# Kernel optimization log

Measured on AMD Instinct MI355X. Metric: run time of the kernel, lower is better.

Reference implementation:

```python
import jax, jax.numpy as jnp
import numpy as np

N_NODES = 100000
N_EDGES = 1600000
IN_DIM, HID_DIM, OUT_DIM = 128, 32, 32
NEG_SLOPE = 0.2  # DGL GATConv default


def setup_inputs() -> dict:
    key = jax.random.key(0)
    ks = jax.random.split(key, 12)
    features = jax.random.normal(ks[0], (N_NODES, IN_DIM), dtype=jnp.float32)
    src = jax.random.randint(ks[1], (N_EDGES,), 0, N_NODES, dtype=jnp.int32)
    dst = jax.random.randint(ks[2], (N_EDGES,), 0, N_NODES, dtype=jnp.int32)
    s1 = 1.0 / np.sqrt(IN_DIM)
    s2 = 1.0 / np.sqrt(HID_DIM)
    W1 = jax.random.normal(ks[3], (IN_DIM, HID_DIM), dtype=jnp.float32) * s1
    al1 = jax.random.normal(ks[4], (HID_DIM,), dtype=jnp.float32) * s2
    ar1 = jax.random.normal(ks[5], (HID_DIM,), dtype=jnp.float32) * s2
    b1 = jnp.zeros((HID_DIM,), dtype=jnp.float32)
    W2 = jax.random.normal(ks[6], (HID_DIM, OUT_DIM), dtype=jnp.float32) * s2
    al2 = jax.random.normal(ks[7], (OUT_DIM,), dtype=jnp.float32) * s2
    ar2 = jax.random.normal(ks[8], (OUT_DIM,), dtype=jnp.float32) * s2
    b2 = jnp.zeros((OUT_DIM,), dtype=jnp.float32)
    return {"features": features, "src": src, "dst": dst,
            "W1": W1, "al1": al1, "ar1": ar1, "b1": b1,
            "W2": W2, "al2": al2, "ar2": ar2, "b2": b2}


def gat_conv(x, W, a_l, a_r, b, src, dst, n_nodes):
    # x: [N, Din] -> h: [N, D]
    h = x @ W
    el = h @ a_l  # [N] per-node left attention logit
    er = h @ a_r  # [N]
    # per-edge score with LeakyReLU (DGL default negative_slope=0.2)
    e = jax.nn.leaky_relu(el[src] + er[dst], negative_slope=NEG_SLOPE)  # [E]
    # segment softmax over edges grouped by destination node
    emax = jax.ops.segment_max(e, dst, num_segments=n_nodes)  # [N]
    ex = jnp.exp(e - emax[dst])  # [E]
    denom = jax.ops.segment_sum(ex, dst, num_segments=n_nodes)  # [N]
    alpha = ex / denom[dst]  # [E], every edge's dst has degree >= 1
    # scatter-weighted aggregation of source features
    out = jax.ops.segment_sum(h[src] * alpha[:, None], dst, num_segments=n_nodes)
    return out + b


def reference(features, src, dst, W1, al1, ar1, b1, W2, al2, ar2, b2):
    n = features.shape[0]
    h = gat_conv(features, W1, al1, ar1, b1, src, dst, n)
    h = jax.nn.elu(h)
    out = gat_conv(h, W2, al2, ar2, b2, src, dst, n)
    return out  # [N, OUT_DIM]
```

## Files before the change

### kernel.cpp

```cpp
#include <hip/hip_runtime.h>
#include <hip/hip_bf16.h>

#define N_NODES 100000
#define N_EDGES 1600000
#define IN_DIM 128
#define HID 32
#define BW 128
#define NBUCK ((N_NODES + BW - 1) / BW)
#define CAP 4096


using bf16x8 = __attribute__((ext_vector_type(8))) short;
using f32x4  = __attribute__((ext_vector_type(4))) float;

__device__ __forceinline__ short f2bf(float f) {
    return __builtin_bit_cast(short, __float2bfloat16(f));
}
__device__ __forceinline__ float bf2f(short s) {
    return __bfloat162float(__builtin_bit_cast(__hip_bfloat16, s));
}

__global__ __launch_bounds__(256) void gemm1_kernel(
    const float* __restrict__ x, const float* __restrict__ W,
    const float* __restrict__ al, const float* __restrict__ ar,
    __hip_bfloat16* __restrict__ h, float* __restrict__ el, float* __restrict__ er,
    int* __restrict__ gcur)
{
    __shared__ float Xs[64][132];
    const int tid = threadIdx.x;
    const int row0 = blockIdx.x * 64;

    const int gid = blockIdx.x * 256 + tid;
    if (gid < NBUCK) gcur[gid] = gid * CAP;

    const int lane = tid & 63, wid = tid >> 6;
    const int l15 = lane & 15, g = lane >> 4;

    bf16x8 bh[4][2], bl[4][2];
    #pragma unroll
    for (int q = 0; q < 4; ++q)
        #pragma unroll
        for (int ct = 0; ct < 2; ++ct)
            #pragma unroll
            for (int j = 0; j < 8; ++j) {
                const float wv = W[(32 * q + 8 * g + j) * HID + ct * 16 + l15];
                const short hi = f2bf(wv);
                bh[q][ct][j] = hi;
                bl[q][ct][j] = f2bf(wv - bf2f(hi));
            }

    #pragma unroll
    for (int i = 0; i < 8; ++i) {
        const int f = tid + 256 * i;
        const int r = f >> 5, c4 = f & 31;
        const int gr = row0 + r;
        float4 v = make_float4(0.f, 0.f, 0.f, 0.f);
        if (gr < N_NODES) v = ((const float4*)x)[(size_t)gr * 32 + c4];
        *(float4*)&Xs[r][c4 * 4] = v;
    }
    __syncthreads();

    const int tile = blockIdx.x * 4 + wid;
    if (tile * 16 >= N_NODES) return;
    const int rl = wid * 16 + l15;

    f32x4 acc0 = {0.f, 0.f, 0.f, 0.f}, acc1 = {0.f, 0.f, 0.f, 0.f};
    #pragma unroll
    for (int q = 0; q < 4; ++q) {
        const float4 xa = *(const float4*)&Xs[rl][32 * q + 8 * g];
        const float4 xb = *(const float4*)&Xs[rl][32 * q + 8 * g + 4];
        const float xs[8] = {xa.x, xa.y, xa.z, xa.w, xb.x, xb.y, xb.z, xb.w};
        bf16x8 ah, alo;
        #pragma unroll
        for (int j = 0; j < 8; ++j) {
            const short hi = f2bf(xs[j]);
            ah[j] = hi;
            alo[j] = f2bf(xs[j] - bf2f(hi));
        }
        acc0 = __builtin_amdgcn_mfma_f32_16x16x32_bf16(ah,  bh[q][0], acc0, 0, 0, 0);
        acc0 = __builtin_amdgcn_mfma_f32_16x16x32_bf16(alo, bh[q][0], acc0, 0, 0, 0);
        acc0 = __builtin_amdgcn_mfma_f32_16x16x32_bf16(ah,  bl[q][0], acc0, 0, 0, 0);
        acc1 = __builtin_amdgcn_mfma_f32_16x16x32_bf16(ah,  bh[q][1], acc1, 0, 0, 0);
        acc1 = __builtin_amdgcn_mfma_f32_16x16x32_bf16(alo, bh[q][1], acc1, 0, 0, 0);
        acc1 = __builtin_amdgcn_mfma_f32_16x16x32_bf16(ah,  bl[q][1], acc1, 0, 0, 0);
    }

    const int grow0 = tile * 16 + 4 * g;
    const float a0 = al[l15], a1 = al[16 + l15];
    const float r0 = ar[l15], r1 = ar[16 + l15];
    float pel[4], per_[4];
    #pragma unroll
    for (int i = 0; i < 4; ++i) {
        const int grow = grow0 + i;
        h[(size_t)grow * HID + l15]      = __float2bfloat16(acc0[i]);
        h[(size_t)grow * HID + 16 + l15] = __float2bfloat16(acc1[i]);
        pel[i]  = acc0[i] * a0 + acc1[i] * a1;
        per_[i] = acc0[i] * r0 + acc1[i] * r1;
    }
    #pragma unroll
    for (int m = 1; m < 16; m <<= 1)
        #pragma unroll
        for (int i = 0; i < 4; ++i) {
            pel[i]  += __shfl_xor(pel[i],  m, 16);
            per_[i] += __shfl_xor(per_[i], m, 16);
        }
    if (l15 == 0)
        #pragma unroll
        for (int i = 0; i < 4; ++i) { el[grow0 + i] = pel[i]; er[grow0 + i] = per_[i]; }
}

__global__ __launch_bounds__(512) void bin_kernel(const int* __restrict__ src,
                                                  const int* __restrict__ dst,
                                                  int* __restrict__ gcur,
                                                  int* __restrict__ pairs)
{
    __shared__ int hist[NBUCK];
    __shared__ int cur[NBUCK];
    const int tid = threadIdx.x;
    for (int i = tid; i < NBUCK; i += 512) hist[i] = 0;
    __syncthreads();

    const int t = blockIdx.x * 512 + tid;
    const bool act = t < N_EDGES / 16;
    int4 sv[4], dv[4];
    if (act) {
        const int4* s4 = (const int4*)src + (size_t)t * 4;
        const int4* d4 = (const int4*)dst + (size_t)t * 4;
        #pragma unroll
        for (int q = 0; q < 4; ++q) { sv[q] = s4[q]; dv[q] = d4[q]; }
        #pragma unroll
        for (int q = 0; q < 4; ++q) {
            atomicAdd(&hist[dv[q].x >> 7], 1); atomicAdd(&hist[dv[q].y >> 7], 1);
            atomicAdd(&hist[dv[q].z >> 7], 1); atomicAdd(&hist[dv[q].w >> 7], 1);
        }
    }
    __syncthreads();
    for (int i = tid; i < NBUCK; i += 512) {
        const int hv = hist[i];
        cur[i] = hv ? atomicAdd(&gcur[i], hv) : 0;
    }
    __syncthreads();
    if (act) {
        #pragma unroll
        for (int q = 0; q < 4; ++q) {
            const int ss[4] = {sv[q].x, sv[q].y, sv[q].z, sv[q].w};
            const int dd[4] = {dv[q].x, dv[q].y, dv[q].z, dv[q].w};
            #pragma unroll
            for (int r = 0; r < 4; ++r) {
                const int slot = atomicAdd(&cur[dd[r] >> 7], 1);
                pairs[slot] = (ss[r] << 7) | (dd[r] & (BW - 1));
            }
        }
    }
}

__global__ __launch_bounds__(256) void lsort_kernel(
    const int* __restrict__ gcur, int* __restrict__ pairs,
    const float* __restrict__ el, const float* __restrict__ er,
    int* __restrict__ deg, int* __restrict__ rowptr, float* __restrict__ w1)
{
    __shared__ int lp[CAP];
    __shared__ int lc[CAP];
    __shared__ int lhist[BW];
    __shared__ int lcur[BW];
    __shared__ float ers[BW];
    __shared__ int w0tot;
    const int tid = threadIdx.x;
    const int b = blockIdx.x;
    const int rbase = b * CAP;
    const int node0 = b * BW;
    int ecnt = gcur[b] - rbase;
    if (ecnt > CAP) ecnt = CAP;
    if (tid < BW) {
        lhist[tid] = 0;
        ers[tid] = (node0 + tid < N_NODES) ? er[node0 + tid] : 0.f;
    }
    __syncthreads();
    for (int i = tid; i < ecnt; i += 256) {
        const int p = pairs[rbase + i];
        lp[i] = p;
        atomicAdd(&lhist[p & (BW - 1)], 1);
    }
    __syncthreads();
    const int lane = tid & 63;
    int v = 0;
    if (tid < BW) v = lhist[tid];
    int pre = v;
    #pragma unroll
    for (int off = 1; off < 64; off <<= 1) {
        const int n = __shfl_up(pre, off, 64);
        if (lane >= off) pre += n;
    }
    if (tid == 63) w0tot = pre;
    __syncthreads();
    if (tid < BW) {
        const int ex = pre - v + (tid >= 64 ? w0tot : 0);
        lcur[tid] = ex;
        const int node = node0 + tid;
        if (node < N_NODES) { deg[node] = v; rowptr[node] = rbase + ex; }
    }
    __syncthreads();
    for (int i = tid; i < ecnt; i += 256) {
        const int p = lp[i];
        const int slot = atomicAdd(&lcur[p & (BW - 1)], 1);
        lc[slot] = p;
    }
    __syncthreads();
    for (int i = tid; i < ecnt; i += 256) {
        const int p = lc[i];
        pairs[rbase + i] = p;
        float sc = el[p >> 7] + ers[p & (BW - 1)];
        sc = sc > 0.f ? sc : 0.2f * sc;
        w1[rbase + i] = __expf(sc);
    }
}

__global__ __launch_bounds__(256) void wcalc_kernel(
    const int* __restrict__ gcur, const int* __restrict__ csr,
    const float* __restrict__ el, const float* __restrict__ er,
    float* __restrict__ w)
{
    __shared__ float ers[BW];
    const int tid = threadIdx.x;
    const int b = blockIdx.x;
    const int rbase = b * CAP;
    const int node0 = b * BW;
    if (tid < BW) ers[tid] = (node0 + tid < N_NODES) ? er[node0 + tid] : 0.f;
    __syncthreads();
    int ecnt = gcur[b] - rbase;
    if (ecnt > CAP) ecnt = CAP;
    for (int i = tid; i < ecnt; i += 256) {
        const int p = csr[rbase + i];
        float sc = el[p >> 7] + ers[p & (BW - 1)];
        sc = sc > 0.f ? sc : 0.2f * sc;
        w[rbase + i] = __expf(sc);
    }
}

template <int MODE>
__global__ __launch_bounds__(256) void gather_kernel(
    const int* __restrict__ rowptr, const int* __restrict__ deg,
    const int* __restrict__ csr, const float* __restrict__ w,
    const __hip_bfloat16* __restrict__ h, const float* __restrict__ bias,
    const float* __restrict__ W2, const float* __restrict__ al2,
    const float* __restrict__ ar2,
    __hip_bfloat16* __restrict__ h2, float* __restrict__ el2,
    float* __restrict__ er2, float* __restrict__ out)
{
    const int tid = threadIdx.x;
    float* W2s = nullptr;
    if constexpr (MODE == 0) {
        __shared__ float W2s_[HID * HID];
        W2s = W2s_;
        ((float4*)W2s)[tid] = ((const float4*)W2)[tid];
        __syncthreads();
    }
    const int node = blockIdx.x * 8 + (tid >> 5);
    const int col = tid & 31;
    const int cnt = deg[node];
    const int start = rowptr[node];
    float acc = 0.f, den = 0.f;
    int j = 0;
    for (; j + 7 < cnt; j += 8) {
        const int p0 = csr[start + j];
        const int p1 = csr[start + j + 1];
        const int p2 = csr[start + j + 2];
        const int p3 = csr[start + j + 3];
        const int p4 = csr[start + j + 4];
        const int p5 = csr[start + j + 5];
        const int p6 = csr[start + j + 6];
        const int p7 = csr[start + j + 7];
        const float w0 = w[start + j];
        const float w1v = w[start + j + 1];
        const float w2v = w[start + j + 2];
        const float w3v = w[start + j + 3];
        const float w4v = w[start + j + 4];
        const float w5v = w[start + j + 5];
        const float w6v = w[start + j + 6];
        const float w7v = w[start + j + 7];
        const float h0 = __bfloat162float(h[(size_t)(p0 >> 7) * HID + col]);
        const float h1 = __bfloat162float(h[(size_t)(p1 >> 7) * HID + col]);
        const float h2v = __bfloat162float(h[(size_t)(p2 >> 7) * HID + col]);
        const float h3 = __bfloat162float(h[(size_t)(p3 >> 7) * HID + col]);
        const float h4 = __bfloat162float(h[(size_t)(p4 >> 7) * HID + col]);
        const float h5 = __bfloat162float(h[(size_t)(p5 >> 7) * HID + col]);
        const float h6 = __bfloat162float(h[(size_t)(p6 >> 7) * HID + col]);
        const float h7 = __bfloat162float(h[(size_t)(p7 >> 7) * HID + col]);
        den += ((w0 + w1v) + (w2v + w3v)) + ((w4v + w5v) + (w6v + w7v));
        acc += (w0 * h0 + w1v * h1 + w2v * h2v + w3v * h3)
             + (w4v * h4 + w5v * h5 + w6v * h6 + w7v * h7);
    }
    for (; j < cnt; ++j) {
        const int p = csr[start + j];
        const float wv = w[start + j];
        den += wv;
        acc += wv * __bfloat162float(h[(size_t)(p >> 7) * HID + col]);
    }

    float v = den > 0.f ? acc / den : 0.f;
    v += bias[col];
    if constexpr (MODE == 0) {
        v = v > 0.f ? v : expm1f(v);
        float hacc = 0.f;
        #pragma unroll
        for (int k = 0; k < HID; ++k)
            hacc += __shfl(v, k, 32) * W2s[k * HID + col];
        h2[(size_t)node * HID + col] = __float2bfloat16(hacc);
        float pel = hacc * al2[col], per = hacc * ar2[col];
        #pragma unroll
        for (int mm = 16; mm > 0; mm >>= 1) {
            pel += __shfl_xor(pel, mm, 32);
            per += __shfl_xor(per, mm, 32);
        }
        if (col == 0) { el2[node] = pel; er2[node] = per; }
    } else {
        out[(size_t)node * HID + col] = v;
    }
}

extern "C" void kernel_launch(void* const* d_in, const int* in_sizes, int n_in,
                              void* d_out, int out_size, void* d_ws, size_t ws_size,
                              hipStream_t stream) {
    const float* features = (const float*)d_in[0];
    const int*   src      = (const int*)d_in[1];
    const int*   dst      = (const int*)d_in[2];
    const float* W1       = (const float*)d_in[3];
    const float* al1      = (const float*)d_in[4];
    const float* ar1      = (const float*)d_in[5];
    const float* b1       = (const float*)d_in[6];
    const float* W2       = (const float*)d_in[7];
    const float* al2      = (const float*)d_in[8];
    const float* ar2      = (const float*)d_in[9];
    const float* b2       = (const float*)d_in[10];
    float* out = (float*)d_out;

    int*  gcur   = (int*)d_ws;
    int*  deg    = gcur + 784;
    int*  rowptr = deg + N_NODES;
    int*  pairs  = rowptr + N_NODES;
    float* wbuf  = (float*)(pairs + NBUCK * CAP);
    __hip_bfloat16* h1 = (__hip_bfloat16*)(wbuf + NBUCK * CAP);
    float* el1 = (float*)(h1 + (size_t)N_NODES * HID);
    float* er1 = el1 + N_NODES;
    __hip_bfloat16* h2 = (__hip_bfloat16*)(er1 + N_NODES);
    float* el2 = (float*)(h2 + (size_t)N_NODES * HID);
    float* er2 = el2 + N_NODES;

    const int NB_E16 = (N_EDGES / 16 + 511) / 512;
    const int NB_G1  = (N_NODES + 63) / 64;

    gemm1_kernel<<<NB_G1, 256, 0, stream>>>(features, W1, al1, ar1,
                                            h1, el1, er1, gcur);
    bin_kernel<<<NB_E16, 512, 0, stream>>>(src, dst, gcur, pairs);
    lsort_kernel<<<NBUCK, 256, 0, stream>>>(gcur, pairs, el1, er1,
                                            deg, rowptr, wbuf);
    gather_kernel<0><<<N_NODES / 8, 256, 0, stream>>>(rowptr, deg, pairs, wbuf,
                                                      h1, b1, W2, al2, ar2,
                                                      h2, el2, er2, nullptr);
    wcalc_kernel<<<NBUCK, 256, 0, stream>>>(gcur, pairs, el2, er2, wbuf);
    gather_kernel<1><<<N_NODES / 8, 256, 0, stream>>>(rowptr, deg, pairs, wbuf,
                                                      h2, b2,
                                                      nullptr, nullptr, nullptr,
                                                      nullptr, nullptr, nullptr, out);
}
```

Before: 255.9 us.

## Stage binned edges in LDS for coalesced writes; split layer-2 GEMM into separate kernel

bin_kernel now sorts each block's 4096 edges into buckets in shared memory, using a wave-level prefix scan for local offsets, then writes them out contiguously per bucket. This is meant to replace scattered global writes with more coalesced ones. The ELU plus W2 projection is moved out of the first gather into a separate gemm2_kernel that goes through an fp32 intermediate buffer x2, which adds a launch and extra global traffic. The gather unroll also drops from 8 to 4.

```diff
diff --git a/kernel.cpp b/kernel.cpp
--- a/kernel.cpp
+++ b/kernel.cpp
@@ -109,18 +109,21 @@
         for (int i = 0; i < 4; ++i) { el[grow0 + i] = pel[i]; er[grow0 + i] = per_[i]; }
 }
 
-__global__ __launch_bounds__(512) void bin_kernel(const int* __restrict__ src,
+__global__ __launch_bounds__(256) void bin_kernel(const int* __restrict__ src,
                                                   const int* __restrict__ dst,
                                                   int* __restrict__ gcur,
                                                   int* __restrict__ pairs)
 {
+    __shared__ int   lp[4096];
+    __shared__ short lb[4096];
     __shared__ int hist[NBUCK];
-    __shared__ int cur[NBUCK];
-    const int tid = threadIdx.x;
-    for (int i = tid; i < NBUCK; i += 512) hist[i] = 0;
-    __syncthreads();
-
-    const int t = blockIdx.x * 512 + tid;
+    __shared__ int lcur[NBUCK];
+    __shared__ int gbase[NBUCK];
+    const int tid = threadIdx.x;
+    for (int i = tid; i < NBUCK; i += 256) hist[i] = 0;
+    __syncthreads();
+
+    const int t = blockIdx.x * 256 + tid;
     const bool act = t < N_EDGES / 16;
     int4 sv[4], dv[4];
     if (act) {
@@ -135,9 +138,24 @@
         }
     }
     __syncthreads();
-    for (int i = tid; i < NBUCK; i += 512) {
+    if (tid < 64) {
+        int carry = 0;
+        for (int c = 0; c < (NBUCK + 63) / 64; ++c) {
+            const int i = c * 64 + tid;
+            const int v = (i < NBUCK) ? hist[i] : 0;
+            int pre = v;
+            #pragma unroll
+            for (int off = 1; off < 64; off <<= 1) {
+                const int n = __shfl_up(pre, off, 64);
+                if (tid >= off) pre += n;
+            }
+            if (i < NBUCK) lcur[i] = carry + pre - v;
+            carry += __shfl(pre, 63, 64);
+        }
+    }
+    for (int i = tid; i < NBUCK; i += 256) {
         const int hv = hist[i];
-        cur[i] = hv ? atomicAdd(&gcur[i], hv) : 0;
+        gbase[i] = hv ? atomicAdd(&gcur[i], hv) : 0;
     }
     __syncthreads();
     if (act) {
@@ -147,10 +165,19 @@
             const int dd[4] = {dv[q].x, dv[q].y, dv[q].z, dv[q].w};
             #pragma unroll
             for (int r = 0; r < 4; ++r) {
-                const int slot = atomicAdd(&cur[dd[r] >> 7], 1);
-                pairs[slot] = (ss[r] << 7) | (dd[r] & (BW - 1));
+                const int b = dd[r] >> 7;
+                const int slot = atomicAdd(&lcur[b], 1);
+                lp[slot] = (ss[r] << 7) | (dd[r] & (BW - 1));
+                lb[slot] = (short)b;
             }
         }
+    }
+    __syncthreads();
+    const int ecB = min(N_EDGES - blockIdx.x * 4096, 4096);
+    for (int i = tid; i < ecB; i += 256) {
+        const int b = lb[i];
+        const int local = i - (lcur[b] - hist[b]);
+        pairs[gbase[b] + local] = lp[i];
     }
 }
 
@@ -242,53 +269,30 @@
     const int* __restrict__ rowptr, const int* __restrict__ deg,
     const int* __restrict__ csr, const float* __restrict__ w,
     const __hip_bfloat16* __restrict__ h, const float* __restrict__ bias,
-    const float* __restrict__ W2, const float* __restrict__ al2,
-    const float* __restrict__ ar2,
-    __hip_bfloat16* __restrict__ h2, float* __restrict__ el2,
-    float* __restrict__ er2, float* __restrict__ out)
-{
-    const int tid = threadIdx.x;
-    float* W2s = nullptr;
-    if constexpr (MODE == 0) {
-        __shared__ float W2s_[HID * HID];
-        W2s = W2s_;
-        ((float4*)W2s)[tid] = ((const float4*)W2)[tid];
-        __syncthreads();
-    }
+    float* __restrict__ out)
+{
+    const int tid = threadIdx.x;
     const int node = blockIdx.x * 8 + (tid >> 5);
     const int col = tid & 31;
     const int cnt = deg[node];
     const int start = rowptr[node];
     float acc = 0.f, den = 0.f;
     int j = 0;
-    for (; j + 7 < cnt; j += 8) {
+    for (; j + 3 < cnt; j += 4) {
         const int p0 = csr[start + j];
         const int p1 = csr[start + j + 1];
         const int p2 = csr[start + j + 2];
         const int p3 = csr[start + j + 3];
-        const int p4 = csr[start + j + 4];
-        const int p5 = csr[start + j + 5];
-        const int p6 = csr[start + j + 6];
-        const int p7 = csr[start + j + 7];
         const float w0 = w[start + j];
         const float w1v = w[start + j + 1];
         const float w2v = w[start + j + 2];
         const float w3v = w[start + j + 3];
-        const float w4v = w[start + j + 4];
-        const float w5v = w[start + j + 5];
-        const float w6v = w[start + j + 6];
-        const float w7v = w[start + j + 7];
         const float h0 = __bfloat162float(h[(size_t)(p0 >> 7) * HID + col]);
         const float h1 = __bfloat162float(h[(size_t)(p1 >> 7) * HID + col]);
         const float h2v = __bfloat162float(h[(size_t)(p2 >> 7) * HID + col]);
         const float h3 = __bfloat162float(h[(size_t)(p3 >> 7) * HID + col]);
-        const float h4 = __bfloat162float(h[(size_t)(p4 >> 7) * HID + col]);
-        const float h5 = __bfloat162float(h[(size_t)(p5 >> 7) * HID + col]);
-        const float h6 = __bfloat162float(h[(size_t)(p6 >> 7) * HID + col]);
-        const float h7 = __bfloat162float(h[(size_t)(p7 >> 7) * HID + col]);
-        den += ((w0 + w1v) + (w2v + w3v)) + ((w4v + w5v) + (w6v + w7v));
-        acc += (w0 * h0 + w1v * h1 + w2v * h2v + w3v * h3)
-             + (w4v * h4 + w5v * h5 + w6v * h6 + w7v * h7);
+        den += (w0 + w1v) + (w2v + w3v);
+        acc += w0 * h0 + w1v * h1 + w2v * h2v + w3v * h3;
     }
     for (; j < cnt; ++j) {
         const int p = csr[start + j];
@@ -296,26 +300,55 @@
         den += wv;
         acc += wv * __bfloat162float(h[(size_t)(p >> 7) * HID + col]);
     }
-
     float v = den > 0.f ? acc / den : 0.f;
     v += bias[col];
-    if constexpr (MODE == 0) {
-        v = v > 0.f ? v : expm1f(v);
-        float hacc = 0.f;
-        #pragma unroll
-        for (int k = 0; k < HID; ++k)
-            hacc += __shfl(v, k, 32) * W2s[k * HID + col];
-        h2[(size_t)node * HID + col] = __float2bfloat16(hacc);
-        float pel = hacc * al2[col], per = hacc * ar2[col];
-        #pragma unroll
-        for (int mm = 16; mm > 0; mm >>= 1) {
-            pel += __shfl_xor(pel, mm, 32);
-            per += __shfl_xor(per, mm, 32);
-        }
-        if (col == 0) { el2[node] = pel; er2[node] = per; }
-    } else {
-        out[(size_t)node * HID + col] = v;
-    }
+    if (MODE == 0) v = v > 0.f ? v : expm1f(v);
+    out[(size_t)node * HID + col] = v;
+}
+
+__global__ __launch_bounds__(256) void gemm2_kernel(
+    const float* __restrict__ x2, const float* __restrict__ W,
+    const float* __restrict__ al, const float* __restrict__ ar,
+    __hip_bfloat16* __restrict__ h, float* __restrict__ el, float* __restrict__ er)
+{
+    __shared__ float Ws[HID][36];
+    __shared__ float Xs[32][36];
+    const int tid = threadIdx.x;
+    const int row0 = blockIdx.x * 32;
+    {
+        const float4 wv = ((const float4*)W)[tid];
+        *(float4*)&Ws[tid >> 3][(tid & 7) * 4] = wv;
+        const float4 xv = ((const float4*)x2)[(size_t)row0 * 8 + tid];
+        *(float4*)&Xs[tid >> 3][(tid & 7) * 4] = xv;
+    }
+    __syncthreads();
+
+    const int r = tid >> 3, cg = tid & 7;
+    const int row = row0 + r;
+    float ax = 0.f, ay = 0.f, az = 0.f, aw = 0.f;
+    #pragma unroll
+    for (int k = 0; k < HID; ++k) {
+        const float xv = Xs[r][k];
+        const float4 wv = *(const float4*)&Ws[k][cg * 4];
+        ax += xv * wv.x; ay += xv * wv.y; az += xv * wv.z; aw += xv * wv.w;
+    }
+
+    ushort4 hp;
+    hp.x = __builtin_bit_cast(unsigned short, __float2bfloat16(ax));
+    hp.y = __builtin_bit_cast(unsigned short, __float2bfloat16(ay));
+    hp.z = __builtin_bit_cast(unsigned short, __float2bfloat16(az));
+    hp.w = __builtin_bit_cast(unsigned short, __float2bfloat16(aw));
+    *(ushort4*)&h[(size_t)row * HID + cg * 4] = hp;
+
+    const int c0 = cg * 4;
+    float pel = ax * al[c0] + ay * al[c0 + 1] + az * al[c0 + 2] + aw * al[c0 + 3];
+    float per = ax * ar[c0] + ay * ar[c0 + 1] + az * ar[c0 + 2] + aw * ar[c0 + 3];
+    #pragma unroll
+    for (int m = 1; m < 8; m <<= 1) {
+        pel += __shfl_xor(pel, m, 8);
+        per += __shfl_xor(per, m, 8);
+    }
+    if (cg == 0) { el[row] = pel; er[row] = per; }
 }
 
 extern "C" void kernel_launch(void* const* d_in, const int* in_sizes, int n_in,
@@ -342,24 +375,23 @@
     __hip_bfloat16* h1 = (__hip_bfloat16*)(wbuf + NBUCK * CAP);
     float* el1 = (float*)(h1 + (size_t)N_NODES * HID);
     float* er1 = el1 + N_NODES;
-    __hip_bfloat16* h2 = (__hip_bfloat16*)(er1 + N_NODES);
+    float* x2  = er1 + N_NODES;
+    __hip_bfloat16* h2 = (__hip_bfloat16*)(x2 + (size_t)N_NODES * HID);
     float* el2 = (float*)(h2 + (size_t)N_NODES * HID);
     float* er2 = el2 + N_NODES;
 
-    const int NB_E16 = (N_EDGES / 16 + 511) / 512;
+    const int NB_E16 = (N_EDGES / 16 + 255) / 256;
     const int NB_G1  = (N_NODES + 63) / 64;
 
     gemm1_kernel<<<NB_G1, 256, 0, stream>>>(features, W1, al1, ar1,
                                             h1, el1, er1, gcur);
-    bin_kernel<<<NB_E16, 512, 0, stream>>>(src, dst, gcur, pairs);
+    bin_kernel<<<NB_E16, 256, 0, stream>>>(src, dst, gcur, pairs);
     lsort_kernel<<<NBUCK, 256, 0, stream>>>(gcur, pairs, el1, er1,
                                             deg, rowptr, wbuf);
     gather_kernel<0><<<N_NODES / 8, 256, 0, stream>>>(rowptr, deg, pairs, wbuf,
-                                                      h1, b1, W2, al2, ar2,
-                                                      h2, el2, er2, nullptr);
+                                                      h1, b1, x2);
+    gemm2_kernel<<<N_NODES / 32, 256, 0, stream>>>(x2, W2, al2, ar2, h2, el2, er2);
     wcalc_kernel<<<NBUCK, 256, 0, stream>>>(gcur, pairs, el2, er2, wbuf);
     gather_kernel<1><<<N_NODES / 8, 256, 0, stream>>>(rowptr, deg, pairs, wbuf,
-                                                      h2, b2,
-                                                      nullptr, nullptr, nullptr,
-                                                      nullptr, nullptr, nullptr, out);
-}
+                                                      h2, b2, out);
+}
```

After: 250.2 us. 1.02x faster.
